# Kernel optimization log

Measured on AMD Instinct MI355X. Metric: run time of the kernel, lower is better.

The kernel has to match this reference:

```python
import jax, jax.numpy as jnp
import numpy as np

N_NODES = 100000
N_EDGES = 3200000
F_IN = 256
HIDDEN = 16
N_CLASSES = 32


def setup_inputs() -> dict:
    key = jax.random.key(0)
    ks = jax.random.split(key, 9)
    x = jax.random.normal(ks[0], (N_NODES, F_IN), dtype=jnp.float32)
    edge_index = jax.random.randint(ks[1], (2, N_EDGES), 0, N_NODES)
    edge_attr = jax.random.uniform(ks[2], (N_EDGES, 1), dtype=jnp.float32)
    s1 = 1.0 / np.sqrt(F_IN)
    W1 = jax.random.normal(ks[3], (2, F_IN, HIDDEN), dtype=jnp.float32) * s1
    root1 = jax.random.normal(ks[4], (F_IN, HIDDEN), dtype=jnp.float32) * s1
    bias1 = jnp.zeros((HIDDEN,), dtype=jnp.float32)
    s2 = 1.0 / np.sqrt(HIDDEN)
    W2 = jax.random.normal(ks[5], (2, HIDDEN, N_CLASSES), dtype=jnp.float32) * s2
    root2 = jax.random.normal(ks[6], (HIDDEN, N_CLASSES), dtype=jnp.float32) * s2
    bias2 = jnp.zeros((N_CLASSES,), dtype=jnp.float32)
    return {"x": x, "edge_attr": edge_attr, "W1": W1, "root1": root1,
            "bias1": bias1, "W2": W2, "root2": root2, "bias2": bias2,
            "edge_index": edge_index}


def spline_conv(x, src, dst, u, W, root, bias):
    """SplineConv, dim=1, kernel_size=2, degree=1, open spline, aggr='mean'.

    With K=2 and degree-1 open splines, v = u*(K-1) = u, so the B-spline basis
    per edge is simply ((1-u), u) over kernel weights W[0], W[1].
    """
    n = x.shape[0]
    # Node-level GEMMs once (cheaper than per-edge F_IN-dim gathers): [2, N, out]
    xs = jnp.einsum('nf,kfo->kno', x, W)
    # Per-edge basis-weighted message from source nodes: [E, out]
    msg = (1.0 - u)[:, None] * xs[0, src] + u[:, None] * xs[1, src]
    agg = jax.ops.segment_sum(msg, dst, num_segments=n)
    cnt = jax.ops.segment_sum(jnp.ones((dst.shape[0],), x.dtype), dst,
                              num_segments=n)
    return agg / jnp.maximum(cnt, 1.0)[:, None] + x @ root + bias


def reference(x, edge_attr, W1, root1, bias1, W2, root2, bias2, edge_index):
    src, dst = edge_index[0], edge_index[1]
    u = jnp.clip(edge_attr[:, 0], 0.0, 1.0)  # pseudo coords in [0, 1]
    # dropout with training=False is identity (eval-mode reference)
    h = jax.nn.elu(spline_conv(x, src, dst, u, W1, root1, bias1))
    out = spline_conv(h, src, dst, u, W2, root2, bias2)
    return jax.nn.log_softmax(out, axis=1)
```

## Files before the change

### kernel.cpp

```cpp
#include <hip/hip_runtime.h>
#include <hip/hip_fp16.h>
#include <math.h>

#define NN 100000
#define NE 3200000
#define FIN 256
#define HID 16
#define NC 32
#define NBUK 782
#define CAP 5120
#define SC_BLOCKS 250
#define SC_TILE 12800
#define SC_EPT 13
#define SK 20

typedef __attribute__((ext_vector_type(8))) short short8;
typedef __attribute__((ext_vector_type(4))) float f32x4;
typedef union { uint4 u; short8 s; } U8;

#define RU(r) ((float)((r) >> 24) * (1.f / 255.f))

__global__ __launch_bounds__(256) void k_prepB(
    const float* __restrict__ W1, const float* __restrict__ root1,
    uint4* __restrict__ Bpk)
{
    int idx = blockIdx.x * 256 + threadIdx.x;
    if (idx >= 1536) return;
    int c = idx & 15, kc = (idx >> 4) & 31, t = idx >> 9;
    unsigned hi[8], lo[8];
    #pragma unroll
    for (int e = 0; e < 8; ++e) {
        int k = kc * 8 + e;
        float v;
        if (t == 0)      v = W1[k * 16 + c];
        else if (t == 1) v = W1[FIN * 16 + k * 16 + c];
        else             v = root1[k * 16 + c];
        unsigned u = __float_as_uint(v);
        unsigned h = u & 0xFFFF0000u;
        float lf = v - __uint_as_float(h);
        hi[e] = h;
        lo[e] = __float_as_uint(lf) & 0xFFFF0000u;
    }
    uint4 H, L;
    H.x = (hi[0] >> 16) | hi[1];  H.y = (hi[2] >> 16) | hi[3];
    H.z = (hi[4] >> 16) | hi[5];  H.w = (hi[6] >> 16) | hi[7];
    L.x = (lo[0] >> 16) | lo[1];  L.y = (lo[2] >> 16) | lo[3];
    L.z = (lo[4] >> 16) | lo[5];  L.w = (lo[6] >> 16) | lo[7];
    Bpk[(size_t)idx * 2]     = H;
    Bpk[(size_t)idx * 2 + 1] = L;
}

__global__ __launch_bounds__(256) void k_gemm1(
    const float* __restrict__ x, const uint4* __restrict__ Bpk,
    const float* __restrict__ bias1,
    __half2* __restrict__ xs1p, __half2* __restrict__ r1h)
{
    int wid = (blockIdx.x << 2) + (threadIdx.x >> 6);
    if (wid >= NN / 16) return;
    int lane = threadIdx.x & 63;
    int c = lane & 15, kcl = lane >> 4;
    int n0 = wid * 16;

    const float* xr = x + (size_t)(n0 + c) * FIN + kcl * 8;
    f32x4 acc0 = {0.f, 0.f, 0.f, 0.f};
    f32x4 acc1 = {0.f, 0.f, 0.f, 0.f};
    f32x4 acc2 = {0.f, 0.f, 0.f, 0.f};

    #define PACK(f0, f1, HO, LO) {                                     \
        unsigned u0 = __float_as_uint(f0), u1 = __float_as_uint(f1);   \
        unsigned h0 = u0 & 0xFFFF0000u, h1 = u1 & 0xFFFF0000u;         \
        HO = (h0 >> 16) | h1;                                          \
        float l0 = (f0) - __uint_as_float(h0);                         \
        float l1 = (f1) - __uint_as_float(h1);                         \
        LO = (__float_as_uint(l0) >> 16) |                             \
             (__float_as_uint(l1) & 0xFFFF0000u); }

    #pragma unroll
    for (int s = 0; s < 8; ++s) {
        float4 a0 = *(const float4*)(xr + s * 32);
        float4 a1 = *(const float4*)(xr + s * 32 + 4);
        U8 ahi, alo;
        PACK(a0.x, a0.y, ahi.u.x, alo.u.x)
        PACK(a0.z, a0.w, ahi.u.y, alo.u.y)
        PACK(a1.x, a1.y, ahi.u.z, alo.u.z)
        PACK(a1.z, a1.w, ahi.u.w, alo.u.w)

        const uint4* bp = Bpk + ((size_t)((s * 4 + kcl) * 16 + c)) * 2;
        U8 bh0, bl0, bh1, bl1, bh2, bl2;
        bh0.u = bp[0];     bl0.u = bp[1];
        bh1.u = bp[1024];  bl1.u = bp[1025];
        bh2.u = bp[2048];  bl2.u = bp[2049];

        acc0 = __builtin_amdgcn_mfma_f32_16x16x32_bf16(ahi.s, bh0.s, acc0, 0, 0, 0);
        acc0 = __builtin_amdgcn_mfma_f32_16x16x32_bf16(alo.s, bh0.s, acc0, 0, 0, 0);
        acc0 = __builtin_amdgcn_mfma_f32_16x16x32_bf16(ahi.s, bl0.s, acc0, 0, 0, 0);
        acc1 = __builtin_amdgcn_mfma_f32_16x16x32_bf16(ahi.s, bh1.s, acc1, 0, 0, 0);
        acc1 = __builtin_amdgcn_mfma_f32_16x16x32_bf16(alo.s, bh1.s, acc1, 0, 0, 0);
        acc1 = __builtin_amdgcn_mfma_f32_16x16x32_bf16(ahi.s, bl1.s, acc1, 0, 0, 0);
        acc2 = __builtin_amdgcn_mfma_f32_16x16x32_bf16(ahi.s, bh2.s, acc2, 0, 0, 0);
        acc2 = __builtin_amdgcn_mfma_f32_16x16x32_bf16(alo.s, bh2.s, acc2, 0, 0, 0);
        acc2 = __builtin_amdgcn_mfma_f32_16x16x32_bf16(ahi.s, bl2.s, acc2, 0, 0, 0);
    }
    #undef PACK

    #pragma unroll
    for (int r = 0; r < 4; ++r) {
        int n = n0 + kcl * 4 + r;
        xs1p[(size_t)n * 16 + c] = __floats2half2_rn(acc0[r], acc1[r]);
    }
    float b = bias1[c];
    #pragma unroll
    for (int r = 0; r < 4; ++r) {
        int n = n0 + kcl * 4 + r;
        float v = acc2[r] + b;
        float vo = __shfl_xor(v, 1, 64);
        if (!(c & 1))
            r1h[(size_t)n * 8 + (c >> 1)] = __floats2half2_rn(v, vo);
    }
}

__global__ __launch_bounds__(1024) void k_binscatter(
    const int* __restrict__ ei, const float* __restrict__ ea,
    int* __restrict__ gcnt, unsigned* __restrict__ rec)
{
    __shared__ int h[NBUK];
    int t = threadIdx.x;
    if (t < NBUK) h[t] = 0;
    __syncthreads();
    int e0 = blockIdx.x * SC_TILE;
    int   dl[SC_EPT];
    int   sl[SC_EPT];
    float ul[SC_EPT];
    #pragma unroll
    for (int k = 0; k < SC_EPT; ++k) {
        int i = t + k * 1024;
        if (i < SC_TILE) {
            dl[k] = ei[NE + e0 + i];
            sl[k] = ei[e0 + i];
            ul[k] = ea[e0 + i];
            atomicAdd(&h[dl[k] >> 7], 1);
        }
    }
    __syncthreads();
    if (t < NBUK) {
        int c = h[t];
        if (c) h[t] = t * CAP + atomicAdd(&gcnt[t], c);
    }
    __syncthreads();
    #pragma unroll
    for (int k = 0; k < SC_EPT; ++k) {
        int i = t + k * 1024;
        if (i < SC_TILE) {
            float u = fminf(fmaxf(ul[k], 0.f), 1.f);
            unsigned uq = (unsigned)(u * 255.f + 0.5f);
            int pos = atomicAdd(&h[dl[k] >> 7], 1);
            rec[pos] = (unsigned)sl[k] | ((unsigned)(dl[k] & 127) << 17)
                     | (uq << 24);
        }
    }
}

__global__ __launch_bounds__(256) void k_sort(
    const int* __restrict__ gcnt, unsigned* __restrict__ rec,
    int* __restrict__ rstart, int* __restrict__ rend)
{
    __shared__ int cnt[128], cur[128], ss[128];
    int t = threadIdx.x;
    if (t < 128) cnt[t] = 0;
    __syncthreads();
    int start = blockIdx.x * CAP, m = gcnt[blockIdx.x];
    unsigned r[SK];
    int nr = 0;
    for (int i = start + t; i < start + m; i += 256) {
        unsigned v = rec[i];
        if (nr < SK) r[nr++] = v;
        atomicAdd(&cnt[(v >> 17) & 127], 1);
    }
    __syncthreads();
    if (t < 128) ss[t] = cnt[t];
    __syncthreads();
    for (int off = 1; off < 128; off <<= 1) {
        int a = (t < 128 && t >= off) ? ss[t - off] : 0;
        __syncthreads();
        if (t < 128) ss[t] += a;
        __syncthreads();
    }
    if (t < 128) {
        int excl = ss[t] - cnt[t];
        cur[t] = excl;
        int n = blockIdx.x * 128 + t;
        if (n < NN) {
            rstart[n] = start + excl;
            rend[n]   = start + excl + cnt[t];
        }
    }
    __syncthreads();
    for (int k = 0; k < nr; ++k) {
        int dl = (int)(r[k] >> 17) & 127;
        int p = atomicAdd(&cur[dl], 1);
        rec[start + p] = r[k];
    }
}

__global__ __launch_bounds__(256) void k_agg1g2(
    const int* __restrict__ rstart, const int* __restrict__ rend,
    const unsigned* __restrict__ rec, const uint2* __restrict__ xs,
    const __half2* __restrict__ r1h, __half2* __restrict__ hh2)
{
    int t = threadIdx.x;
    int nl = t >> 3, j = t & 7;
    int n = blockIdx.x * 32 + nl;
    int s = rstart[n], e = rend[n];
    int d = e - s;
    float a0 = 0.f, a1 = 0.f;

    #define ACC1(r_, g) {                                           \
        float u = RU(r_);                                           \
        float2 f0 = __half22float2(*(const __half2*)&(g).x);        \
        float2 f1 = __half22float2(*(const __half2*)&(g).y);        \
        a0 += (1.f - u) * f0.x + u * f0.y;                          \
        a1 += (1.f - u) * f1.x + u * f1.y; }

    int k = s;
    for (; k + 8 <= e; k += 8) {
        unsigned q[8]; uint2 g[8];
        #pragma unroll
        for (int z = 0; z < 8; ++z) q[z] = rec[k + z];
        #pragma unroll
        for (int z = 0; z < 8; ++z) g[z] = xs[(size_t)(q[z] & 0x1FFFF) * 8 + j];
        #pragma unroll
        for (int z = 0; z < 8; ++z) { ACC1(q[z], g[z]) }
    }
    for (; k < e; ++k) {
        unsigned q = rec[k];
        uint2 g = xs[(size_t)(q & 0x1FFFF) * 8 + j];
        ACC1(q, g)
    }
    #undef ACC1

    float inv = 1.f / fmaxf((float)d, 1.f);
    float2 rr = __half22float2(r1h[(size_t)n * 8 + j]);
    float v0 = a0 * inv + rr.x;
    float v1 = a1 * inv + rr.y;
    v0 = v0 > 0.f ? v0 : expm1f(v0);
    v1 = v1 > 0.f ? v1 : expm1f(v1);
    hh2[(size_t)n * 8 + j] = __floats2half2_rn(v0, v1);
}

__global__ __launch_bounds__(256) void k_agg2(
    const int* __restrict__ rstart, const int* __restrict__ rend,
    const unsigned* __restrict__ rec, const uint2* __restrict__ hh,
    const float* __restrict__ W2, const float* __restrict__ root2,
    const float* __restrict__ bias2, float* __restrict__ out)
{
    __shared__ float wsm[1568];
    __shared__ float ssm[64 * 33];
    __shared__ float hv[64 * 18];
    int t = threadIdx.x;
    for (int i = t; i < 1568; i += 256)
        wsm[i] = (i < 1024) ? W2[i] : (i < 1536 ? root2[i - 1024] : bias2[i - 1536]);

    int nl = t >> 2, j = t & 3;
    int n = blockIdx.x * 64 + nl;
    bool valid = n < NN;
    int s = 0, e = 0;
    if (valid) { s = rstart[n]; e = rend[n]; }
    float s0[4] = {0.f, 0.f, 0.f, 0.f};
    float s1[4] = {0.f, 0.f, 0.f, 0.f};

    #define ACC2(r_, g) {                                           \
        float u = RU(r_);                                           \
        float w0 = 1.f - u;                                         \
        float2 f0 = __half22float2(*(const __half2*)&(g).x);        \
        float2 f1 = __half22float2(*(const __half2*)&(g).y);        \
        s0[0] += w0 * f0.x; s1[0] += u * f0.x;                      \
        s0[1] += w0 * f0.y; s1[1] += u * f0.y;                      \
        s0[2] += w0 * f1.x; s1[2] += u * f1.x;                      \
        s0[3] += w0 * f1.y; s1[3] += u * f1.y; }

    int k = s;
    for (; k + 8 <= e; k += 8) {
        unsigned q[8]; uint2 g[8];
        #pragma unroll
        for (int z = 0; z < 8; ++z) q[z] = rec[k + z];
        #pragma unroll
        for (int z = 0; z < 8; ++z) g[z] = hh[(size_t)(q[z] & 0x1FFFF) * 4 + j];
        #pragma unroll
        for (int z = 0; z < 8; ++z) { ACC2(q[z], g[z]) }
    }
    for (; k < e; ++k) {
        unsigned q = rec[k];
        uint2 g = hh[(size_t)(q & 0x1FFFF) * 4 + j];
        ACC2(q, g)
    }
    #undef ACC2

    float inv = 1.f / fmaxf((float)(e - s), 1.f);
    #pragma unroll
    for (int q2 = 0; q2 < 4; ++q2) {
        ssm[nl * 33 + 4 * j + q2] = s0[q2];
        ssm[nl * 33 + 16 + 4 * j + q2] = s1[q2];
    }
    if (valid) {
        uint2 gh = hh[(size_t)n * 4 + j];
        float2 h0 = __half22float2(*(const __half2*)&gh.x);
        float2 h1 = __half22float2(*(const __half2*)&gh.y);
        hv[nl * 18 + 4 * j]     = h0.x;
        hv[nl * 18 + 4 * j + 1] = h0.y;
        hv[nl * 18 + 4 * j + 2] = h1.x;
        hv[nl * 18 + 4 * j + 3] = h1.y;
    } else {
        hv[nl * 18 + 4 * j]     = 0.f;
        hv[nl * 18 + 4 * j + 1] = 0.f;
        hv[nl * 18 + 4 * j + 2] = 0.f;
        hv[nl * 18 + 4 * j + 3] = 0.f;
    }
    if (j == 0) hv[nl * 18 + 16] = inv;
    __syncthreads();

    float invn = hv[nl * 18 + 16];
    float v[8];
    #pragma unroll
    for (int cc = 0; cc < 8; ++cc) {
        int c = j * 8 + cc;
        float acc = wsm[1536 + c];
        float agg = 0.f;
        #pragma unroll
        for (int kk = 0; kk < 16; ++kk) {
            agg += ssm[nl * 33 + kk] * wsm[kk * 32 + c]
                 + ssm[nl * 33 + 16 + kk] * wsm[512 + kk * 32 + c];
            acc += hv[nl * 18 + kk] * wsm[1024 + kk * 32 + c];
        }
        v[cc] = acc + agg * invn;
    }

    float m = v[0];
    #pragma unroll
    for (int cc = 1; cc < 8; ++cc) m = fmaxf(m, v[cc]);
    #pragma unroll
    for (int off = 1; off < 4; off <<= 1)
        m = fmaxf(m, __shfl_xor(m, off, 4));
    float sm = 0.f;
    #pragma unroll
    for (int cc = 0; cc < 8; ++cc) sm += expf(v[cc] - m);
    #pragma unroll
    for (int off = 1; off < 4; off <<= 1)
        sm += __shfl_xor(sm, off, 4);
    float ls = m + logf(sm);
    if (valid) {
        float4* op = (float4*)(out + (size_t)n * 32 + j * 8);
        op[0] = make_float4(v[0] - ls, v[1] - ls, v[2] - ls, v[3] - ls);
        op[1] = make_float4(v[4] - ls, v[5] - ls, v[6] - ls, v[7] - ls);
    }
}

extern "C" void kernel_launch(void* const* d_in, const int* in_sizes, int n_in,
                              void* d_out, int out_size, void* d_ws, size_t ws_size,
                              hipStream_t stream)
{
    const float* x     = (const float*)d_in[0];
    const float* ea    = (const float*)d_in[1];
    const float* W1    = (const float*)d_in[2];
    const float* root1 = (const float*)d_in[3];
    const float* bias1 = (const float*)d_in[4];
    const float* W2    = (const float*)d_in[5];
    const float* root2 = (const float*)d_in[6];
    const float* bias2 = (const float*)d_in[7];
    const int*   ei    = (const int*)d_in[8];
    float* out = (float*)d_out;

    float* ws = (float*)d_ws;
    __half2* xs1p = (__half2*)ws;
    __half2* r1h  = (__half2*)(ws + (size_t)NN * 16);
    __half2* hh2  = (__half2*)(ws + (size_t)NN * 24);
    unsigned* rec = (unsigned*)(ws + (size_t)NN * 32);
    int*     iws  = (int*)(ws + (size_t)NN * 32 + (size_t)NBUK * CAP);
    int* rstart = iws;
    int* rend   = iws + NN;
    int* gcnt   = iws + 2 * NN;
    uint4* Bpk = (uint4*)(ws + (size_t)NN * 24);

    hipMemsetAsync(gcnt, 0, NBUK * sizeof(int), stream);

    k_prepB<<<6, 256, 0, stream>>>(W1, root1, Bpk);
    k_gemm1<<<(NN / 16 + 3) / 4, 256, 0, stream>>>(x, Bpk, bias1, xs1p, r1h);
    k_binscatter<<<SC_BLOCKS, 1024, 0, stream>>>(ei, ea, gcnt, rec);
    k_sort<<<NBUK, 256, 0, stream>>>(gcnt, rec, rstart, rend);
    k_agg1g2<<<(NN * 8) / 256, 256, 0, stream>>>(rstart, rend, rec,
                                                 (const uint2*)xs1p, r1h, hh2);
    k_agg2<<<(NN + 63) / 64, 256, 0, stream>>>(rstart, rend, rec,
                                               (const uint2*)hh2,
                                               W2, root2, bias2, out);
}
```

Measured before the change: 350.5 us.

## Stage bucket scatter in LDS and widen layer-1 gathers to 16 bytes

The binning kernel now sorts each tile's records by bucket in shared memory, using a block-wide prefix scan, and then writes each bucket's run to global memory contiguously with one wavefront per bucket. This replaces the scattered per-record global stores with coalesced ones. Separately, the layer-1 aggregation gives each node 4 lanes that load uint4 (16 bytes) each instead of 8 lanes loading uint2, so there are fewer, wider gather transactions per edge and more nodes per block. The LDS staging buffer of about 50KB raises LDS use and may limit occupancy in the scatter kernel.

```diff
diff --git a/kernel.cpp b/kernel.cpp
--- a/kernel.cpp
+++ b/kernel.cpp
@@ -123,10 +123,13 @@
     const int* __restrict__ ei, const float* __restrict__ ea,
     int* __restrict__ gcnt, unsigned* __restrict__ rec)
 {
-    __shared__ int h[NBUK];
+    __shared__ unsigned sbuf[SC_TILE];
+    __shared__ int cnt[NBUK], gb[NBUK], cur[NBUK];
+    __shared__ int ss[1024];
     int t = threadIdx.x;
-    if (t < NBUK) h[t] = 0;
-    __syncthreads();
+    if (t < NBUK) cnt[t] = 0;
+    __syncthreads();
+
     int e0 = blockIdx.x * SC_TILE;
     int   dl[SC_EPT];
     int   sl[SC_EPT];
@@ -138,25 +141,48 @@
             dl[k] = ei[NE + e0 + i];
             sl[k] = ei[e0 + i];
             ul[k] = ea[e0 + i];
-            atomicAdd(&h[dl[k] >> 7], 1);
+            atomicAdd(&cnt[dl[k] >> 7], 1);
         }
     }
     __syncthreads();
+
+    int v = (t < NBUK) ? cnt[t] : 0;
+    ss[t] = v;
+    __syncthreads();
+    for (int off = 1; off < 1024; off <<= 1) {
+        int a = (t >= off) ? ss[t - off] : 0;
+        __syncthreads();
+        ss[t] += a;
+        __syncthreads();
+    }
     if (t < NBUK) {
-        int c = h[t];
-        if (c) h[t] = t * CAP + atomicAdd(&gcnt[t], c);
-    }
-    __syncthreads();
+        int lbase = ss[t] - v;
+        cur[t] = lbase;
+        if (v) gb[t] = t * CAP + atomicAdd(&gcnt[t], v) - lbase;
+    }
+    __syncthreads();
+
     #pragma unroll
     for (int k = 0; k < SC_EPT; ++k) {
         int i = t + k * 1024;
         if (i < SC_TILE) {
             float u = fminf(fmaxf(ul[k], 0.f), 1.f);
             unsigned uq = (unsigned)(u * 255.f + 0.5f);
-            int pos = atomicAdd(&h[dl[k] >> 7], 1);
-            rec[pos] = (unsigned)sl[k] | ((unsigned)(dl[k] & 127) << 17)
-                     | (uq << 24);
+            int pos = atomicAdd(&cur[dl[k] >> 7], 1);
+            sbuf[pos] = (unsigned)sl[k] | ((unsigned)(dl[k] & 127) << 17)
+                      | (uq << 24);
         }
+    }
+    __syncthreads();
+
+    int wid = t >> 6, lane = t & 63;
+    for (int b = wid; b < NBUK; b += 16) {
+        int n_ = cnt[b];
+        if (!n_) continue;
+        int lb = cur[b] - n_;
+        int gbb = gb[b];
+        for (int i = lane; i < n_; i += 64)
+            rec[gbb + lb + i] = sbuf[lb + i];
     }
 }
 
@@ -204,47 +230,63 @@
 
 __global__ __launch_bounds__(256) void k_agg1g2(
     const int* __restrict__ rstart, const int* __restrict__ rend,
-    const unsigned* __restrict__ rec, const uint2* __restrict__ xs,
+    const unsigned* __restrict__ rec, const uint4* __restrict__ xs4,
     const __half2* __restrict__ r1h, __half2* __restrict__ hh2)
 {
     int t = threadIdx.x;
-    int nl = t >> 3, j = t & 7;
-    int n = blockIdx.x * 32 + nl;
-    int s = rstart[n], e = rend[n];
+    int nl = t >> 2, j = t & 3;
+    int n = blockIdx.x * 64 + nl;
+    bool valid = n < NN;
+    int s = 0, e = 0;
+    if (valid) { s = rstart[n]; e = rend[n]; }
     int d = e - s;
-    float a0 = 0.f, a1 = 0.f;
+    float a0 = 0.f, a1 = 0.f, a2 = 0.f, a3 = 0.f;
 
     #define ACC1(r_, g) {                                           \
         float u = RU(r_);                                           \
-        float2 f0 = __half22float2(*(const __half2*)&(g).x);        \
-        float2 f1 = __half22float2(*(const __half2*)&(g).y);        \
-        a0 += (1.f - u) * f0.x + u * f0.y;                          \
-        a1 += (1.f - u) * f1.x + u * f1.y; }
+        float w0 = 1.f - u;                                         \
+        const __half2* hp_ = (const __half2*)&(g);                  \
+        float2 f0 = __half22float2(hp_[0]);                         \
+        float2 f1 = __half22float2(hp_[1]);                         \
+        float2 f2 = __half22float2(hp_[2]);                         \
+        float2 f3 = __half22float2(hp_[3]);                         \
+        a0 += w0 * f0.x + u * f0.y;                                 \
+        a1 += w0 * f1.x + u * f1.y;                                 \
+        a2 += w0 * f2.x + u * f2.y;                                 \
+        a3 += w0 * f3.x + u * f3.y; }
 
     int k = s;
     for (; k + 8 <= e; k += 8) {
-        unsigned q[8]; uint2 g[8];
+        unsigned q[8]; uint4 g[8];
         #pragma unroll
         for (int z = 0; z < 8; ++z) q[z] = rec[k + z];
         #pragma unroll
-        for (int z = 0; z < 8; ++z) g[z] = xs[(size_t)(q[z] & 0x1FFFF) * 8 + j];
+        for (int z = 0; z < 8; ++z) g[z] = xs4[(size_t)(q[z] & 0x1FFFF) * 4 + j];
         #pragma unroll
         for (int z = 0; z < 8; ++z) { ACC1(q[z], g[z]) }
     }
     for (; k < e; ++k) {
         unsigned q = rec[k];
-        uint2 g = xs[(size_t)(q & 0x1FFFF) * 8 + j];
+        uint4 g = xs4[(size_t)(q & 0x1FFFF) * 4 + j];
         ACC1(q, g)
     }
     #undef ACC1
 
-    float inv = 1.f / fmaxf((float)d, 1.f);
-    float2 rr = __half22float2(r1h[(size_t)n * 8 + j]);
-    float v0 = a0 * inv + rr.x;
-    float v1 = a1 * inv + rr.y;
-    v0 = v0 > 0.f ? v0 : expm1f(v0);
-    v1 = v1 > 0.f ? v1 : expm1f(v1);
-    hh2[(size_t)n * 8 + j] = __floats2half2_rn(v0, v1);
+    if (valid) {
+        float inv = 1.f / fmaxf((float)d, 1.f);
+        float2 rrA = __half22float2(r1h[(size_t)n * 8 + 2 * j]);
+        float2 rrB = __half22float2(r1h[(size_t)n * 8 + 2 * j + 1]);
+        float v0 = a0 * inv + rrA.x;
+        float v1 = a1 * inv + rrA.y;
+        float v2 = a2 * inv + rrB.x;
+        float v3 = a3 * inv + rrB.y;
+        v0 = v0 > 0.f ? v0 : expm1f(v0);
+        v1 = v1 > 0.f ? v1 : expm1f(v1);
+        v2 = v2 > 0.f ? v2 : expm1f(v2);
+        v3 = v3 > 0.f ? v3 : expm1f(v3);
+        hh2[(size_t)n * 8 + 2 * j]     = __floats2half2_rn(v0, v1);
+        hh2[(size_t)n * 8 + 2 * j + 1] = __floats2half2_rn(v2, v3);
+    }
 }
 
 __global__ __launch_bounds__(256) void k_agg2(
@@ -386,8 +428,8 @@
     k_gemm1<<<(NN / 16 + 3) / 4, 256, 0, stream>>>(x, Bpk, bias1, xs1p, r1h);
     k_binscatter<<<SC_BLOCKS, 1024, 0, stream>>>(ei, ea, gcnt, rec);
     k_sort<<<NBUK, 256, 0, stream>>>(gcnt, rec, rstart, rend);
-    k_agg1g2<<<(NN * 8) / 256, 256, 0, stream>>>(rstart, rend, rec,
-                                                 (const uint2*)xs1p, r1h, hh2);
+    k_agg1g2<<<(NN + 63) / 64, 256, 0, stream>>>(rstart, rend, rec,
+                                                 (const uint4*)xs1p, r1h, hh2);
     k_agg2<<<(NN + 63) / 64, 256, 0, stream>>>(rstart, rend, rec,
                                                (const uint2*)hh2,
                                                W2, root2, bias2, out);
```

After: 349.9 us. About the same (-0.2%).
